# Optimization experiments

Measured on AMD Instinct MI355X. Metric: run time of the kernel, lower is better.

The kernel has to match this reference:

```python
import jax, jax.numpy as jnp
import numpy as np
import math

S, B, D = 1024, 8, 512
H = 8
HD = D // H
DFF = 2048
NUM_BUCKETS = 32
MAX_DISTANCE = 128
LN_EPS = 1e-5


def setup_inputs() -> dict:
    key = jax.random.key(0)
    ks = jax.random.split(key, 12)
    s = 0.02
    return {
        "x": jax.random.normal(ks[0], (S, B, D), jnp.float32),
        "attn_mask": jnp.zeros((S, S), jnp.float32),
        "in_proj_w": jax.random.normal(ks[1], (3 * D, D), jnp.float32) * s,
        "in_proj_b": jnp.zeros((3 * D,), jnp.float32),
        "out_proj_w": jax.random.normal(ks[2], (D, D), jnp.float32) * s,
        "out_proj_b": jnp.zeros((D,), jnp.float32),
        "lin1_w": jax.random.normal(ks[3], (DFF, D), jnp.float32) * s,
        "lin1_b": jnp.zeros((DFF,), jnp.float32),
        "lin2_w": jax.random.normal(ks[4], (D, DFF), jnp.float32) * s,
        "lin2_b": jnp.zeros((D,), jnp.float32),
        "ln1_w": jnp.ones((D,), jnp.float32),
        "ln1_b": jnp.zeros((D,), jnp.float32),
        "ln2_w": jnp.ones((D,), jnp.float32),
        "ln2_b": jnp.zeros((D,), jnp.float32),
        "rel_emb": jax.random.normal(ks[5], (NUM_BUCKETS, H), jnp.float32) * s,
    }


def _relative_position_bucket(relative_position, num_buckets=NUM_BUCKETS, max_distance=MAX_DISTANCE):
    # bidirectional=True path (encoder)
    nb = num_buckets // 2
    rel_buckets = (relative_position > 0).astype(jnp.int32) * nb
    rp = jnp.abs(relative_position)
    max_exact = nb // 2
    is_small = rp < max_exact
    rp_safe = jnp.maximum(rp, 1)  # avoid log(0); masked by is_small below
    rp_large = max_exact + (
        jnp.log(rp_safe.astype(jnp.float32) / max_exact)
        / math.log(max_distance / max_exact)
        * (nb - max_exact)
    ).astype(jnp.int32)
    rp_large = jnp.minimum(rp_large, nb - 1)
    return rel_buckets + jnp.where(is_small, rp, rp_large)


def _compute_bias(rel_emb, q_len, k_len):
    ctx = jnp.arange(q_len, dtype=jnp.int32)[:, None]
    mem = jnp.arange(k_len, dtype=jnp.int32)[None, :]
    buckets = _relative_position_bucket(mem - ctx)          # [S, S]
    values = rel_emb[buckets]                                # [S, S, H]
    return jnp.transpose(values, (2, 0, 1))                  # [H, S, S]


def _layer_norm(x, w, b):
    mu = jnp.mean(x, axis=-1, keepdims=True)
    var = jnp.mean(jnp.square(x - mu), axis=-1, keepdims=True)
    return (x - mu) * jax.lax.rsqrt(var + LN_EPS) * w + b


def reference(x, attn_mask, in_proj_w, in_proj_b, out_proj_w, out_proj_b,
              lin1_w, lin1_b, lin2_w, lin2_b, ln1_w, ln1_b, ln2_w, ln2_b, rel_emb):
    s, b, d = x.shape
    # qkv projection (torch Linear: y = x W^T + b)
    qkv = x @ in_proj_w.T + in_proj_b                         # [S, B, 3D]
    q, k, v = jnp.split(qkv, 3, axis=-1)

    def to_bhsd(t):
        return jnp.transpose(t.reshape(s, b, H, HD), (1, 2, 0, 3))  # [B, H, S, HD]

    q, k, v = to_bhsd(q), to_bhsd(k), to_bhsd(v)
    scores = jnp.einsum("bhqd,bhkd->bhqk", q, k) / math.sqrt(HD)

    bias = _compute_bias(rel_emb, s, s)                       # [H, S, S]
    mask_bias = attn_mask[None, :, :] + bias                  # [H, S, S]
    attn = jax.nn.softmax(scores + mask_bias[None], axis=-1)  # [B, H, S, S]

    o = jnp.einsum("bhqk,bhkd->bhqd", attn, v)                # [B, H, S, HD]
    o = jnp.transpose(o, (2, 0, 1, 3)).reshape(s, b, d)       # [S, B, D]
    o = o @ out_proj_w.T + out_proj_b

    # post-norm (norm_first=False)
    y = _layer_norm(x + o, ln1_w, ln1_b)
    ff = jax.nn.relu(y @ lin1_w.T + lin1_b) @ lin2_w.T + lin2_b
    return _layer_norm(y + ff, ln2_w, ln2_b)
```

## Files before the change

kernel.cpp:

```cpp
#include <hip/hip_runtime.h>
#include <hip/hip_bf16.h>


#define S_LEN 1024
#define BATCH 8
#define DMODEL 512
#define NHEAD 8
#define HDIM 64
#define DFF 2048
#define NROWS (S_LEN * BATCH)

typedef __bf16 bf16x8 __attribute__((ext_vector_type(8)));
typedef short  s16x4  __attribute__((ext_vector_type(4)));
typedef float  f32x4  __attribute__((ext_vector_type(4)));

__device__ __forceinline__ void gload16(const void* g, void* l) {
    __builtin_amdgcn_global_load_lds(
        (const __attribute__((address_space(1))) void*)g,
        (__attribute__((address_space(3))) void*)l, 16, 0, 0);
}

__global__ __launch_bounds__(256)
void prep_embc_kernel(const float* __restrict__ x,
                      const float* __restrict__ wq, const float* __restrict__ wo,
                      const float* __restrict__ w1, const float* __restrict__ w2,
                      __hip_bfloat16* __restrict__ xb, __hip_bfloat16* __restrict__ wqb,
                      __hip_bfloat16* __restrict__ wob, __hip_bfloat16* __restrict__ w1b,
                      __hip_bfloat16* __restrict__ w2b,
                      const float* __restrict__ mask,
                      const float* __restrict__ rel_emb,
                      __hip_bfloat16* __restrict__ embC) {
    if (blockIdx.x < 7168) {
        const int NX = NROWS * DMODEL / 4;
        const int NQ = 3 * DMODEL * DMODEL / 4;
        const int NO = DMODEL * DMODEL / 4;
        const int N1 = DFF * DMODEL / 4;
        int i = blockIdx.x * 256 + threadIdx.x;
        const float* src; __hip_bfloat16* dst; int off;
        if (i < NX)                         { src = x;  dst = xb;  off = i; }
        else if ((i -= NX) < NQ)            { src = wq; dst = wqb; off = i; }
        else if ((i -= NQ) < NO)            { src = wo; dst = wob; off = i; }
        else if ((i -= NO) < N1)            { src = w1; dst = w1b; off = i; }
        else if ((i -= N1) < N1)            { src = w2; dst = w2b; off = i; }
        else return;
        float4 v = *(const float4*)(src + (size_t)off * 4);
        union { s16x4 s; __hip_bfloat16 b[4]; } u;
        u.b[0] = __float2bfloat16(v.x); u.b[1] = __float2bfloat16(v.y);
        u.b[2] = __float2bfloat16(v.z); u.b[3] = __float2bfloat16(v.w);
        *(s16x4*)(dst + (size_t)off * 4) = u.s;
    } else {
        int tid = (blockIdx.x - 7168) * 256 + threadIdx.x;
        int h  = tid >> 16;
        int r1 = tid & 65535;
        int qt = r1 >> 12;
        int w  = (r1 >> 10) & 3;
        int kb = (r1 >> 6) & 15;
        int lane = r1 & 63;
        int q = qt * 64 + w * 16 + (lane & 15);
        __hip_bfloat16 ov[16];
#pragma unroll
        for (int j = 0; j < 16; ++j) {
            int c = j >> 2, e = j & 3;
            int k = kb * 64 + c * 16 + (lane >> 4) * 4 + e;
            int rel = k - q;
            int bucket = (rel > 0) ? 16 : 0;
            int rp = rel < 0 ? -rel : rel;
            int v;
            if (rp < 8)          v = rp;
            else if (rp < 12)    v = 8;
            else if (rp < 16)    v = 9;
            else if (rp < 23)    v = 10;
            else if (rp < 32)    v = 11;
            else if (rp < 46)    v = 12;
            else if (rp < 64)    v = 13;
            else if (rp < 91)    v = 14;
            else                 v = 15;
            float bt = rel_emb[(bucket + v) * NHEAD + h];
            ov[j] = __float2bfloat16(__expf(mask[(size_t)q * S_LEN + k] + bt));
        }
        *(uint4*)(embC + (size_t)tid * 16) = *(uint4*)&ov[0];
        *(uint4*)(embC + (size_t)tid * 16 + 8) = *(uint4*)&ov[8];
    }
}

#define TSTR 136

template <int MODE, bool RELU>
__global__ __launch_bounds__(256, 4)
void gemm_tile(const __hip_bfloat16* __restrict__ Ab,
               const __hip_bfloat16* __restrict__ Wb,
               const float* __restrict__ bias,
               void* __restrict__ outv,
               int N, int M, int Kloop, int Kstride) {
    const int id = blockIdx.x;
    int by, bx, bz;
    if (MODE == 0) { bz = id >> 8; int rem = id & 255; by = rem & 63; bx = rem >> 6; }
    else           { bz = 0; by = id & 63; bx = id >> 6; }
    const int w = threadIdx.x >> 6;
    const int lane = threadIdx.x & 63;
    const int m16 = lane & 15;
    const int quad = lane >> 4;
    const int row0 = by * 128;
    const int col0 = bx * 128;
    const int kbase = bz * Kloop;
    const int rowbase = (w >> 1) * 64;
    const int colbase = (w & 1) * 64;

    __shared__ __align__(16) __bf16 SH[128 * TSTR];
    __bf16* As = SH;
    __bf16* Bs = SH + 128 * 64;

    const __bf16* Ap = (const __bf16*)Ab;
    const __bf16* Wp = (const __bf16*)Wb;

    const int a_row_in_grp = lane >> 3;
    const int kb_sw = (lane & 7) ^ (lane >> 3);

    f32x4 acc[4][4];
#pragma unroll
    for (int c = 0; c < 4; ++c)
#pragma unroll
        for (int r = 0; r < 4; ++r) acc[c][r] = f32x4{0, 0, 0, 0};

    for (int k0 = 0; k0 < Kloop; k0 += 64) {
#pragma unroll
        for (int i = 0; i < 4; ++i) {
            int grp = w * 4 + i;
            int row = grp * 8 + a_row_in_grp;
            gload16(Ap + (size_t)(row0 + row) * Kstride + kbase + k0 + kb_sw * 8,
                    (void*)(As + grp * 512));
            gload16(Wp + (size_t)(col0 + row) * Kstride + kbase + k0 + kb_sw * 8,
                    (void*)(Bs + grp * 512));
        }
        __syncthreads();

#pragma unroll
        for (int kk = 0; kk < 2; ++kk) {
            bf16x8 af[4], bfr[4];
            int slot = (kk * 4 + quad) ^ (m16 & 7);
#pragma unroll
            for (int r = 0; r < 4; ++r)
                af[r] = *(const bf16x8*)(As + (rowbase + r * 16 + m16) * 64 + slot * 8);
#pragma unroll
            for (int c = 0; c < 4; ++c)
                bfr[c] = *(const bf16x8*)(Bs + (colbase + c * 16 + m16) * 64 + slot * 8);
#pragma unroll
            for (int c = 0; c < 4; ++c)
#pragma unroll
                for (int r = 0; r < 4; ++r)
                    acc[c][r] = __builtin_amdgcn_mfma_f32_16x16x32_bf16(
                        af[r], bfr[c], acc[c][r], 0, 0, 0);
        }
        __syncthreads();
    }

    if (MODE == 0) {
#pragma unroll
        for (int c = 0; c < 4; ++c) {
            int col = col0 + colbase + c * 16 + m16;
            float bv = (bz != 0) ? 0.f : bias[col];
#pragma unroll
            for (int r = 0; r < 4; ++r)
#pragma unroll
                for (int e = 0; e < 4; ++e) {
                    int row = row0 + rowbase + r * 16 + quad * 4 + e;
                    ((float*)outv)[(size_t)bz * N * M + (size_t)row * M + col] =
                        acc[c][r][e] + bv;
                }
        }
    } else {
        __hip_bfloat16* T = (__hip_bfloat16*)SH;
#pragma unroll
        for (int c = 0; c < 4; ++c) {
            int colL = colbase + c * 16 + m16;
            float bv = bias[col0 + colL];
#pragma unroll
            for (int r = 0; r < 4; ++r) {
                int rowL = rowbase + r * 16 + quad * 4;
#pragma unroll
                for (int e = 0; e < 4; ++e) {
                    float v = acc[c][r][e] + bv;
                    if (RELU) v = fmaxf(v, 0.f);
                    T[(rowL + e) * TSTR + colL] = __float2bfloat16(v);
                }
            }
        }
        __syncthreads();

        const int u = threadIdx.x;
        if (MODE == 1 || col0 < 1024) {
            int rowL = u >> 1, half = u & 1;
            int gcol = col0 + half * 64;
            size_t base;
            if (MODE == 1) {
                base = (size_t)(row0 + rowL) * M + gcol;
            } else {
                int sect = gcol >> 9, h = (gcol >> 6) & 7;
                int s = (row0 + rowL) >> 3, bb = (row0 + rowL) & 7;
                base = ((size_t)(sect * 64 + bb * 8 + h) * S_LEN + s) * HDIM;
            }
            __hip_bfloat16* op = (__hip_bfloat16*)outv + base;
#pragma unroll
            for (int j = 0; j < 8; ++j)
                *(uint4*)(op + j * 8) = *(const uint4*)&T[rowL * TSTR + half * 64 + j * 8];
        } else {
#pragma unroll
            for (int t2 = 0; t2 < 4; ++t2) {
                int pairIdx = u * 4 + t2;
                int bb = pairIdx >> 7;
                int cl = pairIdx & 127;
                int gcol = col0 + cl;
                int h = (gcol >> 6) & 7, d = gcol & 63;
                unsigned short tv[16];
#pragma unroll
                for (int k = 0; k < 16; ++k)
                    tv[k] = *(const unsigned short*)&T[(bb + 8 * k) * TSTR + cl];
                size_t base = (size_t)(128 + bb * 8 + h) * (S_LEN * HDIM)
                            + (size_t)d * S_LEN + by * 16;
                *(uint4*)((__hip_bfloat16*)outv + base)     = *(uint4*)&tv[0];
                *(uint4*)((__hip_bfloat16*)outv + base + 8) = *(uint4*)&tv[8];
            }
        }
    }
}

__global__ __launch_bounds__(256)
void gemm64_db(const __hip_bfloat16* __restrict__ Ab,
               const __hip_bfloat16* __restrict__ Wb,
               const float* __restrict__ bias,
               float* __restrict__ outf,
               int N, int M, int K) {
    const int id = blockIdx.x;
    const int by = id & 63, bx = id >> 6;
    const int w = threadIdx.x >> 6;
    const int lane = threadIdx.x & 63;
    const int m16 = lane & 15;
    const int quad = lane >> 4;
    const int row0 = by * 128;
    const int col0 = bx * 64;
    const int rowbase = w * 32;

    __shared__ __align__(16) __bf16 As[2][128 * 64];
    __shared__ __align__(16) __bf16 Bs[2][64 * 64];

    const __bf16* Ap = (const __bf16*)Ab;
    const __bf16* Wp = (const __bf16*)Wb;

    const int a_row_in_grp = lane >> 3;
    const int kb_sw = (lane & 7) ^ (lane >> 3);

    auto stage = [&](int k0, int p) {
#pragma unroll
        for (int i = 0; i < 4; ++i) {
            int grp = w * 4 + i;
            int row = grp * 8 + a_row_in_grp;
            gload16(Ap + (size_t)(row0 + row) * K + k0 + kb_sw * 8,
                    (void*)(&As[p][grp * 512]));
        }
#pragma unroll
        for (int i = 0; i < 2; ++i) {
            int grp = w * 2 + i;
            int row = grp * 8 + a_row_in_grp;
            gload16(Wp + (size_t)(col0 + row) * K + k0 + kb_sw * 8,
                    (void*)(&Bs[p][grp * 512]));
        }
    };

    f32x4 acc[4][2];
#pragma unroll
    for (int c = 0; c < 4; ++c)
#pragma unroll
        for (int r = 0; r < 2; ++r) acc[c][r] = f32x4{0, 0, 0, 0};

    stage(0, 0);
    __syncthreads();

    int p = 0;
    for (int k0 = 0; k0 < K; k0 += 64, p ^= 1) {
        if (k0 + 64 < K) stage(k0 + 64, p ^ 1);
#pragma unroll
        for (int kk = 0; kk < 2; ++kk) {
            bf16x8 af[2], bfr[4];
            int slot = (kk * 4 + quad) ^ (m16 & 7);
#pragma unroll
            for (int r = 0; r < 2; ++r)
                af[r] = *(const bf16x8*)(&As[p][(rowbase + r * 16 + m16) * 64 + slot * 8]);
#pragma unroll
            for (int c = 0; c < 4; ++c)
                bfr[c] = *(const bf16x8*)(&Bs[p][(c * 16 + m16) * 64 + slot * 8]);
#pragma unroll
            for (int c = 0; c < 4; ++c)
#pragma unroll
                for (int r = 0; r < 2; ++r)
                    acc[c][r] = __builtin_amdgcn_mfma_f32_16x16x32_bf16(
                        af[r], bfr[c], acc[c][r], 0, 0, 0);
        }
        __syncthreads();
    }

#pragma unroll
    for (int c = 0; c < 4; ++c) {
        int col = col0 + c * 16 + m16;
        float bv = bias[col];
#pragma unroll
        for (int r = 0; r < 2; ++r)
#pragma unroll
            for (int e = 0; e < 4; ++e) {
                int row = row0 + rowbase + r * 16 + quad * 4 + e;
                outf[(size_t)row * M + col] = acc[c][r][e] + bv;
            }
    }
}

__global__ __launch_bounds__(256, 2)
void attn_mfma(const __hip_bfloat16* __restrict__ qkv_bhsd,
               const __hip_bfloat16* __restrict__ embC,
               __hip_bfloat16* __restrict__ o) {
    const int id = blockIdx.x;
    const int h = id & 7;
    const int qb = (id >> 3) & 7;
    const int b = id >> 6;
    const int bh = b * 8 + h;
    const int q0 = qb * 128;
    const int t = threadIdx.x;
    const int w = t >> 6, lane = t & 63, m16 = lane & 15, quad = lane >> 4;

    const __bf16* Qb  = (const __bf16*)qkv_bhsd + (size_t)bh * (S_LEN * HDIM);
    const __bf16* Kb  = (const __bf16*)qkv_bhsd + (size_t)(64 + bh) * (S_LEN * HDIM);
    const __bf16* VTg = (const __bf16*)qkv_bhsd + (size_t)(128 + bh) * (S_LEN * HDIM);
    const int qtA = qb * 2, qtB = qtA + 1;
    const __hip_bfloat16* ecA =
        embC + ((((size_t)h * 16 + qtA) * 4 + w) * 16) * 1024 + (size_t)lane * 16;
    const __hip_bfloat16* ecB =
        embC + ((((size_t)h * 16 + qtB) * 4 + w) * 16) * 1024 + (size_t)lane * 16;

    __shared__ __align__(16) __bf16 Ks[2][64 * 64];
    __shared__ __align__(16) __bf16 Vs[2][64 * 64];
    __shared__ __align__(16) __bf16 P[4][2][16 * 64];

    const int r_in = lane >> 3;
    const int kb_sw = (lane & 7) ^ r_in;

    auto stage = [&](int kc, int p) {
#pragma unroll
        for (int i = 0; i < 2; ++i) {
            int grp = w * 2 + i;
            gload16(Kb + (size_t)(kc + grp * 8 + r_in) * HDIM + kb_sw * 8,
                    (void*)(&Ks[p][grp * 512]));
            gload16(VTg + (size_t)(grp * 8 + r_in) * S_LEN + kc + kb_sw * 8,
                    (void*)(&Vs[p][grp * 512]));
        }
    };

    bf16x8 aQ0A, aQ1A, aQ0B, aQ1B;
    {
        const __bf16* qpA = Qb + (size_t)(q0 + w * 16 + m16) * HDIM + quad * 8;
        const __bf16* qpB = qpA + (size_t)64 * HDIM;
        bf16x8 t0 = *(const bf16x8*)qpA;
        bf16x8 t1 = *(const bf16x8*)(qpA + 32);
        bf16x8 t2 = *(const bf16x8*)qpB;
        bf16x8 t3 = *(const bf16x8*)(qpB + 32);
#pragma unroll
        for (int j = 0; j < 8; ++j) {
            t0[j] = (__bf16)((float)t0[j] * 0.125f);
            t1[j] = (__bf16)((float)t1[j] * 0.125f);
            t2[j] = (__bf16)((float)t2[j] * 0.125f);
            t3[j] = (__bf16)((float)t3[j] * 0.125f);
        }
        aQ0A = t0; aQ1A = t1; aQ0B = t2; aQ1B = t3;
    }

    f32x4 accOTA[4] = {f32x4{0,0,0,0}, f32x4{0,0,0,0}, f32x4{0,0,0,0}, f32x4{0,0,0,0}};
    f32x4 accOTB[4] = {f32x4{0,0,0,0}, f32x4{0,0,0,0}, f32x4{0,0,0,0}, f32x4{0,0,0,0}};
    float lpartA = 0.f, lpartB = 0.f;

    stage(0, 0);
    __syncthreads();

    int p = 0;
    for (int kc = 0; kc < S_LEN; kc += 64, p ^= 1) {
        if (kc + 64 < S_LEN) stage(kc + 64, p ^ 1);

        union { uint4 u[2]; __hip_bfloat16 e[16]; } evA, evB;
        evA.u[0] = *(const uint4*)(ecA + (size_t)(kc >> 6) * 1024);
        evA.u[1] = *(const uint4*)(ecA + (size_t)(kc >> 6) * 1024 + 8);
        evB.u[0] = *(const uint4*)(ecB + (size_t)(kc >> 6) * 1024);
        evB.u[1] = *(const uint4*)(ecB + (size_t)(kc >> 6) * 1024 + 8);

        f32x4 accTA[4] = {f32x4{0,0,0,0}, f32x4{0,0,0,0}, f32x4{0,0,0,0}, f32x4{0,0,0,0}};
        f32x4 accTB[4] = {f32x4{0,0,0,0}, f32x4{0,0,0,0}, f32x4{0,0,0,0}, f32x4{0,0,0,0}};
        const int sub = (m16 >> 3) * 512 + (m16 & 7) * 64;
        const int s0 = (quad ^ (m16 & 7)) * 8;
        const int s1 = ((4 + quad) ^ (m16 & 7)) * 8;
#pragma unroll
        for (int c = 0; c < 4; ++c) {
            const __bf16* kr = &Ks[p][c * 1024 + sub];
            bf16x8 b0 = *(const bf16x8*)(kr + s0);
            bf16x8 b1 = *(const bf16x8*)(kr + s1);
            accTA[c] = __builtin_amdgcn_mfma_f32_16x16x32_bf16(b0, aQ0A, accTA[c], 0, 0, 0);
            accTA[c] = __builtin_amdgcn_mfma_f32_16x16x32_bf16(b1, aQ1A, accTA[c], 0, 0, 0);
            accTB[c] = __builtin_amdgcn_mfma_f32_16x16x32_bf16(b0, aQ0B, accTB[c], 0, 0, 0);
            accTB[c] = __builtin_amdgcn_mfma_f32_16x16x32_bf16(b1, aQ1B, accTB[c], 0, 0, 0);
        }

#pragma unroll
        for (int c = 0; c < 4; ++c) {
            union { s16x4 s; __hip_bfloat16 bb[4]; } uA, uB;
#pragma unroll
            for (int e = 0; e < 4; ++e) {
                float pvA = __expf(accTA[c][e]) * __bfloat162float(evA.e[c * 4 + e]);
                float pvB = __expf(accTB[c][e]) * __bfloat162float(evB.e[c * 4 + e]);
                lpartA += pvA; lpartB += pvB;
                uA.bb[e] = __float2bfloat16(pvA);
                uB.bb[e] = __float2bfloat16(pvB);
            }
            int blk = (c * 2 + (quad >> 1)) ^ (m16 & 7);
            *(s16x4*)&P[w][0][m16 * 64 + blk * 8 + (quad & 1) * 4] = uA.s;
            *(s16x4*)&P[w][1][m16 * 64 + blk * 8 + (quad & 1) * 4] = uB.s;
        }

        bf16x8 pb0A = *(const bf16x8*)&P[w][0][m16 * 64 + ((quad) ^ (m16 & 7)) * 8];
        bf16x8 pb1A = *(const bf16x8*)&P[w][0][m16 * 64 + ((4 + quad) ^ (m16 & 7)) * 8];
        bf16x8 pb0B = *(const bf16x8*)&P[w][1][m16 * 64 + ((quad) ^ (m16 & 7)) * 8];
        bf16x8 pb1B = *(const bf16x8*)&P[w][1][m16 * 64 + ((4 + quad) ^ (m16 & 7)) * 8];

#pragma unroll
        for (int dt = 0; dt < 4; ++dt) {
            const __bf16* vr = &Vs[p][dt * 1024 + sub];
            bf16x8 v0 = *(const bf16x8*)(vr + s0);
            bf16x8 v1 = *(const bf16x8*)(vr + s1);
            accOTA[dt] = __builtin_amdgcn_mfma_f32_16x16x32_bf16(v0, pb0A, accOTA[dt], 0, 0, 0);
            accOTA[dt] = __builtin_amdgcn_mfma_f32_16x16x32_bf16(v1, pb1A, accOTA[dt], 0, 0, 0);
            accOTB[dt] = __builtin_amdgcn_mfma_f32_16x16x32_bf16(v0, pb0B, accOTB[dt], 0, 0, 0);
            accOTB[dt] = __builtin_amdgcn_mfma_f32_16x16x32_bf16(v1, pb1B, accOTB[dt], 0, 0, 0);
        }

        __syncthreads();
    }

    float lA = lpartA, lB = lpartB;
    lA += __shfl_xor(lA, 16); lA += __shfl_xor(lA, 32);
    lB += __shfl_xor(lB, 16); lB += __shfl_xor(lB, 32);
    float invA = 1.f / lA, invB = 1.f / lB;

    {
        __bf16* Tw = &P[w][0][0];
        const int qr = lane >> 2, ch = lane & 3;
#pragma unroll
        for (int tile = 0; tile < 2; ++tile) {
            const f32x4* accp = tile ? accOTB : accOTA;
            float inv = tile ? invB : invA;
#pragma unroll
            for (int dt = 0; dt < 4; ++dt) {
                union { s16x4 s; __hip_bfloat16 bb4[4]; } uu;
#pragma unroll
                for (int e = 0; e < 4; ++e)
                    uu.bb4[e] = __float2bfloat16(accp[dt][e] * inv);
                *(s16x4*)&Tw[m16 * 72 + dt * 16 + quad * 4] = uu.s;
            }
            asm volatile("s_waitcnt lgkmcnt(0)" ::: "memory");
            __builtin_amdgcn_sched_barrier(0);
            int qg = q0 + tile * 64 + w * 16 + qr;
            __hip_bfloat16* op = o + ((size_t)qg * BATCH + b) * DMODEL
                               + h * HDIM + ch * 16;
            *(uint4*)op       = *(const uint4*)&Tw[qr * 72 + ch * 16];
            *(uint4*)(op + 8) = *(const uint4*)&Tw[qr * 72 + ch * 16 + 8];
            asm volatile("s_waitcnt lgkmcnt(0)" ::: "memory");
            __builtin_amdgcn_sched_barrier(0);
        }
    }
}

__global__ __launch_bounds__(64)
void ln_kernel(const float* __restrict__ resid,
               const float* __restrict__ gin,
               const float* __restrict__ gin2,
               const float* __restrict__ w,
               const float* __restrict__ b,
               float* __restrict__ outf,
               __hip_bfloat16* __restrict__ outb) {
    const int row = blockIdx.x;
    const int lane = threadIdx.x;
    const float* rp = resid + (size_t)row * DMODEL;
    const float* gp = gin + (size_t)row * DMODEL;

    float4 v[2];
    float s = 0.f, s2 = 0.f;
#pragma unroll
    for (int i = 0; i < 2; ++i) {
        int d = i * 256 + lane * 4;
        float4 a = *(const float4*)(rp + d);
        float4 g = *(const float4*)(gp + d);
        a.x += g.x; a.y += g.y; a.z += g.z; a.w += g.w;
        if (gin2) {
            float4 g2 = *(const float4*)(gin2 + (size_t)row * DMODEL + d);
            a.x += g2.x; a.y += g2.y; a.z += g2.z; a.w += g2.w;
        }
        v[i] = a;
        s += a.x + a.y + a.z + a.w;
        s2 += a.x * a.x + a.y * a.y + a.z * a.z + a.w * a.w;
    }
#pragma unroll
    for (int off = 32; off; off >>= 1) {
        s  += __shfl_xor(s, off);
        s2 += __shfl_xor(s2, off);
    }
    float mu = s * (1.f / DMODEL);
    float var = s2 * (1.f / DMODEL) - mu * mu;
    float rs = rsqrtf(var + 1e-5f);
#pragma unroll
    for (int i = 0; i < 2; ++i) {
        int d = i * 256 + lane * 4;
        float4 wv = *(const float4*)(w + d);
        float4 bv = *(const float4*)(b + d);
        float4 y;
        y.x = (v[i].x - mu) * rs * wv.x + bv.x;
        y.y = (v[i].y - mu) * rs * wv.y + bv.y;
        y.z = (v[i].z - mu) * rs * wv.z + bv.z;
        y.w = (v[i].w - mu) * rs * wv.w + bv.w;
        *(float4*)(outf + (size_t)row * DMODEL + d) = y;
        if (outb) {
            union { s16x4 s4; __hip_bfloat16 e[4]; } u;
            u.e[0] = __float2bfloat16(y.x); u.e[1] = __float2bfloat16(y.y);
            u.e[2] = __float2bfloat16(y.z); u.e[3] = __float2bfloat16(y.w);
            *(s16x4*)(outb + (size_t)row * DMODEL + d) = u.s4;
        }
    }
}

extern "C" void kernel_launch(void* const* d_in, const int* in_sizes, int n_in,
                              void* d_out, int out_size, void* d_ws, size_t ws_size,
                              hipStream_t stream) {
    const float* x          = (const float*)d_in[0];
    const float* attn_mask  = (const float*)d_in[1];
    const float* in_proj_w  = (const float*)d_in[2];
    const float* in_proj_b  = (const float*)d_in[3];
    const float* out_proj_w = (const float*)d_in[4];
    const float* out_proj_b = (const float*)d_in[5];
    const float* lin1_w     = (const float*)d_in[6];
    const float* lin1_b     = (const float*)d_in[7];
    const float* lin2_w     = (const float*)d_in[8];
    const float* lin2_b     = (const float*)d_in[9];
    const float* ln1_w      = (const float*)d_in[10];
    const float* ln1_b      = (const float*)d_in[11];
    const float* ln2_w      = (const float*)d_in[12];
    const float* ln2_b      = (const float*)d_in[13];
    const float* rel_emb    = (const float*)d_in[14];

    char* ws = (char*)d_ws;
    size_t off = 0;
    auto alloc = [&](size_t bytes) {
        char* p = ws + off;
        off += (bytes + 255) / 256 * 256;
        return (void*)p;
    };
    __hip_bfloat16* embt  = (__hip_bfloat16*)alloc((size_t)NHEAD * S_LEN * S_LEN * 2);
    __hip_bfloat16* wqkvb = (__hip_bfloat16*)alloc((size_t)3 * DMODEL * DMODEL * 2);
    __hip_bfloat16* wob   = (__hip_bfloat16*)alloc((size_t)DMODEL * DMODEL * 2);
    __hip_bfloat16* w1b   = (__hip_bfloat16*)alloc((size_t)DFF * DMODEL * 2);
    __hip_bfloat16* w2b   = (__hip_bfloat16*)alloc((size_t)DMODEL * DFF * 2);
    __hip_bfloat16* xb    = (__hip_bfloat16*)alloc((size_t)NROWS * DMODEL * 2);
    __hip_bfloat16* qkvb  = (__hip_bfloat16*)alloc((size_t)3 * 64 * S_LEN * HDIM * 2);
    __hip_bfloat16* o     = (__hip_bfloat16*)alloc((size_t)NROWS * DMODEL * 2);
    float* tmp            = (float*)alloc((size_t)2 * NROWS * DMODEL * 4);
    float* yf             = (float*)alloc((size_t)NROWS * DMODEL * 4);
    __hip_bfloat16* yb    = (__hip_bfloat16*)alloc((size_t)NROWS * DMODEL * 2);
    __hip_bfloat16* ffb   = (__hip_bfloat16*)alloc((size_t)NROWS * DFF * 2);

    float* out = (float*)d_out;
    float* tmp2 = tmp + (size_t)NROWS * DMODEL;

    prep_embc_kernel<<<dim3(9216), 256, 0, stream>>>(
        x, in_proj_w, out_proj_w, lin1_w, lin2_w, xb, wqkvb, wob, w1b, w2b,
        attn_mask, rel_emb, embt);

    gemm_tile<2, false><<<dim3(768), 256, 0, stream>>>(
        xb, wqkvb, in_proj_b, qkvb, NROWS, 3 * DMODEL, DMODEL, DMODEL);

    attn_mfma<<<dim3(512), 256, 0, stream>>>(qkvb, embt, o);

    gemm64_db<<<dim3(512), 256, 0, stream>>>(
        o, wob, out_proj_b, tmp, NROWS, DMODEL, DMODEL);

    ln_kernel<<<dim3(NROWS), 64, 0, stream>>>(x, tmp, nullptr, ln1_w, ln1_b, yf, yb);

    gemm_tile<1, true><<<dim3(1024), 256, 0, stream>>>(
        yb, w1b, lin1_b, ffb, NROWS, DFF, DMODEL, DMODEL);

    gemm_tile<0, false><<<dim3(512), 256, 0, stream>>>(
        ffb, w2b, lin2_b, tmp, NROWS, DMODEL, DFF / 2, DFF);

    ln_kernel<<<dim3(NROWS), 64, 0, stream>>>(yf, tmp, tmp2, ln2_w, ln2_b, out, nullptr);
}
```

Measured before the change: 260.2 us.

## Fuse weight casts and bias-table build into QKV GEMM launch, share mask exp across heads

```diff
diff --git a/kernel.cpp b/kernel.cpp
--- a/kernel.cpp
+++ b/kernel.cpp
@@ -20,44 +20,50 @@
         (__attribute__((address_space(3))) void*)l, 16, 0, 0);
 }
 
+__device__ __forceinline__ void cast4(const float* __restrict__ src,
+                                      __hip_bfloat16* __restrict__ dst, int off) {
+    float4 v = *(const float4*)(src + (size_t)off * 4);
+    union { s16x4 s; __hip_bfloat16 b[4]; } u;
+    u.b[0] = __float2bfloat16(v.x); u.b[1] = __float2bfloat16(v.y);
+    u.b[2] = __float2bfloat16(v.z); u.b[3] = __float2bfloat16(v.w);
+    *(s16x4*)(dst + (size_t)off * 4) = u.s;
+}
+
 __global__ __launch_bounds__(256)
-void prep_embc_kernel(const float* __restrict__ x,
-                      const float* __restrict__ wq, const float* __restrict__ wo,
-                      const float* __restrict__ w1, const float* __restrict__ w2,
-                      __hip_bfloat16* __restrict__ xb, __hip_bfloat16* __restrict__ wqb,
-                      __hip_bfloat16* __restrict__ wob, __hip_bfloat16* __restrict__ w1b,
-                      __hip_bfloat16* __restrict__ w2b,
-                      const float* __restrict__ mask,
-                      const float* __restrict__ rel_emb,
-                      __hip_bfloat16* __restrict__ embC) {
-    if (blockIdx.x < 7168) {
-        const int NX = NROWS * DMODEL / 4;
-        const int NQ = 3 * DMODEL * DMODEL / 4;
-        const int NO = DMODEL * DMODEL / 4;
-        const int N1 = DFF * DMODEL / 4;
-        int i = blockIdx.x * 256 + threadIdx.x;
-        const float* src; __hip_bfloat16* dst; int off;
-        if (i < NX)                         { src = x;  dst = xb;  off = i; }
-        else if ((i -= NX) < NQ)            { src = wq; dst = wqb; off = i; }
-        else if ((i -= NQ) < NO)            { src = wo; dst = wob; off = i; }
-        else if ((i -= NO) < N1)            { src = w1; dst = w1b; off = i; }
-        else if ((i -= N1) < N1)            { src = w2; dst = w2b; off = i; }
-        else return;
-        float4 v = *(const float4*)(src + (size_t)off * 4);
-        union { s16x4 s; __hip_bfloat16 b[4]; } u;
-        u.b[0] = __float2bfloat16(v.x); u.b[1] = __float2bfloat16(v.y);
-        u.b[2] = __float2bfloat16(v.z); u.b[3] = __float2bfloat16(v.w);
-        *(s16x4*)(dst + (size_t)off * 4) = u.s;
-    } else {
-        int tid = (blockIdx.x - 7168) * 256 + threadIdx.x;
-        int h  = tid >> 16;
-        int r1 = tid & 65535;
-        int qt = r1 >> 12;
-        int w  = (r1 >> 10) & 3;
-        int kb = (r1 >> 6) & 15;
-        int lane = r1 & 63;
+void prep_cast_kernel(const float* __restrict__ x, const float* __restrict__ wq,
+                      __hip_bfloat16* __restrict__ xb,
+                      __hip_bfloat16* __restrict__ wqb) {
+    const int NX = NROWS * DMODEL / 4;
+    const int NQ = 3 * DMODEL * DMODEL / 4;
+    int i = blockIdx.x * 256 + threadIdx.x;
+    if (i < NX)              cast4(x, xb, i);
+    else if ((i -= NX) < NQ) cast4(wq, wqb, i);
+}
+
+#define TSTR 136
+
+__global__ __launch_bounds__(256, 4)
+void qkv_fused(const __hip_bfloat16* __restrict__ Ab,
+               const __hip_bfloat16* __restrict__ Wb,
+               const float* __restrict__ bias,
+               __hip_bfloat16* __restrict__ outq,
+               const float* __restrict__ wo, const float* __restrict__ w1,
+               const float* __restrict__ w2,
+               __hip_bfloat16* __restrict__ wob, __hip_bfloat16* __restrict__ w1b,
+               __hip_bfloat16* __restrict__ w2b,
+               const float* __restrict__ mask,
+               const float* __restrict__ rel_emb,
+               __hip_bfloat16* __restrict__ embC) {
+    __shared__ __align__(16) __bf16 SH[128 * TSTR];
+
+    if (blockIdx.x >= 3072) {
+        float* ebt = (float*)SH;
+        ebt[threadIdx.x] = __expf(rel_emb[threadIdx.x]);
+        __syncthreads();
+        int t2 = (blockIdx.x - 3072) * 256 + threadIdx.x;
+        int qt = t2 >> 12, w = (t2 >> 10) & 3, kb = (t2 >> 6) & 15, lane = t2 & 63;
         int q = qt * 64 + w * 16 + (lane & 15);
-        __hip_bfloat16 ov[16];
+        float em[16]; int bv[16];
 #pragma unroll
         for (int j = 0; j < 16; ++j) {
             int c = j >> 2, e = j & 3;
@@ -75,15 +81,135 @@
             else if (rp < 64)    v = 13;
             else if (rp < 91)    v = 14;
             else                 v = 15;
-            float bt = rel_emb[(bucket + v) * NHEAD + h];
-            ov[j] = __float2bfloat16(__expf(mask[(size_t)q * S_LEN + k] + bt));
-        }
-        *(uint4*)(embC + (size_t)tid * 16) = *(uint4*)&ov[0];
-        *(uint4*)(embC + (size_t)tid * 16 + 8) = *(uint4*)&ov[8];
-    }
-}
-
-#define TSTR 136
+            bv[j] = (bucket + v) * NHEAD;
+            em[j] = __expf(mask[(size_t)q * S_LEN + k]);
+        }
+#pragma unroll
+        for (int h = 0; h < NHEAD; ++h) {
+            __hip_bfloat16 ov[16];
+#pragma unroll
+            for (int j = 0; j < 16; ++j)
+                ov[j] = __float2bfloat16(em[j] * ebt[bv[j] + h]);
+            size_t idx = ((((size_t)h * 16 + qt) * 4 + w) * 16 + kb) * 64 + lane;
+            *(uint4*)(embC + idx * 16)     = *(uint4*)&ov[0];
+            *(uint4*)(embC + idx * 16 + 8) = *(uint4*)&ov[8];
+        }
+        return;
+    }
+    if (blockIdx.x >= 768) {
+        const int NO = DMODEL * DMODEL / 4;
+        const int N1 = DFF * DMODEL / 4;
+        int i = (blockIdx.x - 768) * 256 + threadIdx.x;
+        if (i < NO)              cast4(wo, wob, i);
+        else if ((i -= NO) < N1) cast4(w1, w1b, i);
+        else                     cast4(w2, w2b, i - N1);
+        return;
+    }
+
+    const int id = blockIdx.x;
+    const int by = id & 63, bx = id >> 6;
+    const int w = threadIdx.x >> 6;
+    const int lane = threadIdx.x & 63;
+    const int m16 = lane & 15;
+    const int quad = lane >> 4;
+    const int row0 = by * 128;
+    const int col0 = bx * 128;
+    const int rowbase = (w >> 1) * 64;
+    const int colbase = (w & 1) * 64;
+    const int K = DMODEL;
+
+    __bf16* As = SH;
+    __bf16* Bs = SH + 128 * 64;
+
+    const __bf16* Ap = (const __bf16*)Ab;
+    const __bf16* Wp = (const __bf16*)Wb;
+
+    const int a_row_in_grp = lane >> 3;
+    const int kb_sw = (lane & 7) ^ (lane >> 3);
+
+    f32x4 acc[4][4];
+#pragma unroll
+    for (int c = 0; c < 4; ++c)
+#pragma unroll
+        for (int r = 0; r < 4; ++r) acc[c][r] = f32x4{0, 0, 0, 0};
+
+    for (int k0 = 0; k0 < K; k0 += 64) {
+#pragma unroll
+        for (int i = 0; i < 4; ++i) {
+            int grp = w * 4 + i;
+            int row = grp * 8 + a_row_in_grp;
+            gload16(Ap + (size_t)(row0 + row) * K + k0 + kb_sw * 8,
+                    (void*)(As + grp * 512));
+            gload16(Wp + (size_t)(col0 + row) * K + k0 + kb_sw * 8,
+                    (void*)(Bs + grp * 512));
+        }
+        __syncthreads();
+
+#pragma unroll
+        for (int kk = 0; kk < 2; ++kk) {
+            bf16x8 af[4], bfr[4];
+            int slot = (kk * 4 + quad) ^ (m16 & 7);
+#pragma unroll
+            for (int r = 0; r < 4; ++r)
+                af[r] = *(const bf16x8*)(As + (rowbase + r * 16 + m16) * 64 + slot * 8);
+#pragma unroll
+            for (int c = 0; c < 4; ++c)
+                bfr[c] = *(const bf16x8*)(Bs + (colbase + c * 16 + m16) * 64 + slot * 8);
+#pragma unroll
+            for (int c = 0; c < 4; ++c)
+#pragma unroll
+                for (int r = 0; r < 4; ++r)
+                    acc[c][r] = __builtin_amdgcn_mfma_f32_16x16x32_bf16(
+                        af[r], bfr[c], acc[c][r], 0, 0, 0);
+        }
+        __syncthreads();
+    }
+
+    __hip_bfloat16* T = (__hip_bfloat16*)SH;
+#pragma unroll
+    for (int c = 0; c < 4; ++c) {
+        int colL = colbase + c * 16 + m16;
+        float bv = bias[col0 + colL];
+#pragma unroll
+        for (int r = 0; r < 4; ++r) {
+            int rowL = rowbase + r * 16 + quad * 4;
+#pragma unroll
+            for (int e = 0; e < 4; ++e)
+                T[(rowL + e) * TSTR + colL] = __float2bfloat16(acc[c][r][e] + bv);
+        }
+    }
+    __syncthreads();
+
+    const int u = threadIdx.x;
+    if (col0 < 1024) {
+        int rowL = u >> 1, half = u & 1;
+        int gcol = col0 + half * 64;
+        int sect = gcol >> 9, h = (gcol >> 6) & 7;
+        int s = (row0 + rowL) >> 3, bb = (row0 + rowL) & 7;
+        size_t base = ((size_t)(sect * 64 + bb * 8 + h) * S_LEN + s) * HDIM;
+        __hip_bfloat16* op = outq + base;
+#pragma unroll
+        for (int j = 0; j < 8; ++j)
+            *(uint4*)(op + j * 8) = *(const uint4*)&T[rowL * TSTR + half * 64 + j * 8];
+    } else {
+#pragma unroll
+        for (int t2 = 0; t2 < 4; ++t2) {
+            int pairIdx = u * 4 + t2;
+            int bb = pairIdx >> 7;
+            int cl = pairIdx & 127;
+            int gcol = col0 + cl;
+            int h = (gcol >> 6) & 7, d = gcol & 63;
+            unsigned short tv[16];
+#pragma unroll
+            for (int k = 0; k < 16; ++k)
+                tv[k] = *(const unsigned short*)&T[(bb + 8 * k) * TSTR + cl];
+            size_t base = (size_t)(128 + bb * 8 + h) * (S_LEN * HDIM)
+                        + (size_t)d * S_LEN + by * 16;
+            *(uint4*)(outq + base)     = *(uint4*)&tv[0];
+            *(uint4*)(outq + base + 8) = *(uint4*)&tv[8];
+        }
+    }
+}
 
 template <int MODE, bool RELU>
 __global__ __launch_bounds__(256, 4)
@@ -186,41 +312,13 @@
             }
         }
         __syncthreads();
-
         const int u = threadIdx.x;
-        if (MODE == 1 || col0 < 1024) {
-            int rowL = u >> 1, half = u & 1;
-            int gcol = col0 + half * 64;
-            size_t base;
-            if (MODE == 1) {
-                base = (size_t)(row0 + rowL) * M + gcol;
-            } else {
-                int sect = gcol >> 9, h = (gcol >> 6) & 7;
-                int s = (row0 + rowL) >> 3, bb = (row0 + rowL) & 7;
-                base = ((size_t)(sect * 64 + bb * 8 + h) * S_LEN + s) * HDIM;
-            }
-            __hip_bfloat16* op = (__hip_bfloat16*)outv + base;
-#pragma unroll
-            for (int j = 0; j < 8; ++j)
-                *(uint4*)(op + j * 8) = *(const uint4*)&T[rowL * TSTR + half * 64 + j * 8];
-        } else {
-#pragma unroll
-            for (int t2 = 0; t2 < 4; ++t2) {
-                int pairIdx = u * 4 + t2;
-                int bb = pairIdx >> 7;
-                int cl = pairIdx & 127;
-                int gcol = col0 + cl;
-                int h = (gcol >> 6) & 7, d = gcol & 63;
-                unsigned short tv[16];
-#pragma unroll
-                for (int k = 0; k < 16; ++k)
-                    tv[k] = *(const unsigned short*)&T[(bb + 8 * k) * TSTR + cl];
-                size_t base = (size_t)(128 + bb * 8 + h) * (S_LEN * HDIM)
-                            + (size_t)d * S_LEN + by * 16;
-                *(uint4*)((__hip_bfloat16*)outv + base)     = *(uint4*)&tv[0];
-                *(uint4*)((__hip_bfloat16*)outv + base + 8) = *(uint4*)&tv[8];
-            }
-        }
+        int rowL = u >> 1, half = u & 1;
+        __hip_bfloat16* op = (__hip_bfloat16*)outv
+                           + (size_t)(row0 + rowL) * M + col0 + half * 64;
+#pragma unroll
+        for (int j = 0; j < 8; ++j)
+            *(uint4*)(op + j * 8) = *(const uint4*)&T[rowL * TSTR + half * 64 + j * 8];
     }
 }
 
@@ -570,12 +668,12 @@
     float* out = (float*)d_out;
     float* tmp2 = tmp + (size_t)NROWS * DMODEL;
 
-    prep_embc_kernel<<<dim3(9216), 256, 0, stream>>>(
-        x, in_proj_w, out_proj_w, lin1_w, lin2_w, xb, wqkvb, wob, w1b, w2b,
+    prep_cast_kernel<<<dim3(4864), 256, 0, stream>>>(x, in_proj_w, xb, wqkvb);
+
+    qkv_fused<<<dim3(3328), 256, 0, stream>>>(
+        xb, wqkvb, in_proj_b, qkvb,
+        out_proj_w, lin1_w, lin2_w, wob, w1b, w2b,
         attn_mask, rel_emb, embt);
-
-    gemm_tile<2, false><<<dim3(768), 256, 0, stream>>>(
-        xb, wqkvb, in_proj_b, qkvb, NROWS, 3 * DMODEL, DMODEL, DMODEL);
 
     attn_mfma<<<dim3(512), 256, 0, stream>>>(qkvb, embt, o);
 
```

After: 262.7 us. No clear change (+1.0%).
